# Kernel tuning notes

Hardware: AMD Instinct MI355X
Metric: run time of the kernel (lower is better)

## Reference

```python
import jax, jax.numpy as jnp
import numpy as np

N = 50000          # num_entities
R = 16             # num_relations
D = 128            # embedding_dim
B = 4              # num_blocks
d = D // B         # block size (32)
E = 800000         # num edges


def setup_inputs() -> dict:
    key = jax.random.key(0)
    ks = jax.random.split(key, 9)
    s = 1.0 / np.sqrt(D)
    return {
        "edge_index": jax.random.randint(ks[0], (2, E), 0, N),
        "edge_type": jax.random.randint(ks[1], (E,), 0, R),
        "node_emb": jax.random.normal(ks[2], (N, D), jnp.float32) * s,
        "W1": jax.random.normal(ks[3], (R, B, d, d), jnp.float32) * s,
        "root1": jax.random.normal(ks[4], (D, D), jnp.float32) * s,
        "bias1": jax.random.normal(ks[5], (D,), jnp.float32) * 0.01,
        "W2": jax.random.normal(ks[6], (R, B, d, d), jnp.float32) * s,
        "root2": jax.random.normal(ks[7], (D, D), jnp.float32) * s,
        "bias2": jax.random.normal(ks[8], (D,), jnp.float32) * 0.01,
    }


def _rgcn_conv(x, src, dst, et, W, root, bias):
    # x: [N, D]; W: [R, B, d, d] block-diagonal per-relation weights.
    n = x.shape[0]
    # Transform every node under every relation (cheaper than gathering
    # per-edge weight blocks): [R, N, B, d] -> [R, N, D]
    allR = jnp.einsum('nbi,rbio->rnbo', x.reshape(n, B, d), W).reshape(R, n, D)
    msg = allR[et, src]                                   # [E, D] gather
    # Per-relation mean normalization 1/c_{i,r} (PyG RGCNConv aggr='mean'
    # applied per relation): count edges per (dst, relation) pair.
    seg = dst * R + et
    cnt = jax.ops.segment_sum(jnp.ones_like(et, x.dtype), seg, num_segments=n * R)
    norm = 1.0 / jnp.maximum(cnt[seg], 1.0)               # [E]
    agg = jax.ops.segment_sum(msg * norm[:, None], dst, num_segments=n)
    return agg + x @ root + bias


def reference(edge_index, edge_type, node_emb, W1, root1, bias1, W2, root2, bias2):
    src, dst = edge_index[0], edge_index[1]
    h = _rgcn_conv(node_emb, src, dst, edge_type, W1, root1, bias1)
    h = jax.nn.relu(h)  # dropout is identity in eval mode
    return _rgcn_conv(h, src, dst, edge_type, W2, root2, bias2)
```

## Files before the change

kernel.cpp:

```cpp
#include <hip/hip_runtime.h>
#include <hip/hip_bf16.h>

#define N_NODES 50000
#define N_REL   16
#define DIM     128
#define NBLK    4
#define BS      32
#define N_EDGES 800000
#define NSEG    (N_NODES * N_REL)
#define SCAN_BLK 1024
#define N_SCAN_BLKS ((NSEG + SCAN_BLK - 1) / SCAN_BLK)
#define NWT     (N_NODES / 16)

typedef __attribute__((ext_vector_type(8))) short s8v;
typedef __attribute__((ext_vector_type(8))) unsigned short u8v;
typedef __attribute__((ext_vector_type(4))) float f4v;

__device__ __forceinline__ float bf2f(unsigned short u) {
    return __uint_as_float(((unsigned int)u) << 16);
}
__device__ __forceinline__ unsigned short f2bfbits(float f) {
    unsigned int u = __float_as_uint(f);
    return (unsigned short)((u + 0x7fffu + ((u >> 16) & 1u)) >> 16);
}

__global__ __launch_bounds__(256) void count_kernel(const int* __restrict__ src,
                                                    const int* __restrict__ dst,
                                                    const int* __restrict__ et,
                                                    int* __restrict__ cnt,
                                                    int* __restrict__ used, int E) {
    int e = blockIdx.x * 256 + threadIdx.x;
    if (e < E) {
        int r = et[e];
        atomicAdd(&cnt[dst[e] * N_REL + r], 1);
        used[r * N_NODES + src[e]] = 1;
    }
}

__global__ __launch_bounds__(256) void scan1j_kernel(const int* __restrict__ cnt,
                                                     const int* __restrict__ used,
                                                     int* __restrict__ off,
                                                     int* __restrict__ cmap,
                                                     int2* __restrict__ bsum, int M) {
    const int t = threadIdx.x;
    const int base = blockIdx.x * SCAN_BLK + t * 4;
    int c[4], u[4];
#pragma unroll
    for (int i = 0; i < 4; ++i) {
        int idx = base + i;
        c[i] = (idx < M) ? cnt[idx] : 0;
        u[i] = (idx < M) ? used[idx] : 0;
    }
    int cs = c[0] + c[1] + c[2] + c[3];
    int us = u[0] + u[1] + u[2] + u[3];
    const int lane = t & 63, wid = t >> 6;
    int cinc = cs, uinc = us;
    for (int d = 1; d < 64; d <<= 1) {
        int a = __shfl_up(cinc, d, 64);
        int b = __shfl_up(uinc, d, 64);
        if (lane >= d) { cinc += a; uinc += b; }
    }
    __shared__ int cw[5], uw[5];
    if (lane == 63) { cw[wid] = cinc; uw[wid] = uinc; }
    __syncthreads();
    if (t == 0) {
        int a = 0, b = 0;
        for (int w = 0; w < 4; ++w) {
            int x = cw[w]; cw[w] = a; a += x;
            int y = uw[w]; uw[w] = b; b += y;
        }
        cw[4] = a; uw[4] = b;
    }
    __syncthreads();
    int cex = cinc - cs + cw[wid];
    int uex = uinc - us + uw[wid];
#pragma unroll
    for (int i = 0; i < 4; ++i) {
        int idx = base + i;
        if (idx < M) { off[idx] = cex; cmap[idx] = uex; }
        cex += c[i]; uex += u[i];
    }
    if (t == 0) bsum[blockIdx.x] = make_int2(cw[4], uw[4]);
}

__global__ __launch_bounds__(1024) void scan2j_kernel(int2* __restrict__ bsum, int nb) {
    const int t = threadIdx.x;
    int2 s = (t < nb) ? bsum[t] : make_int2(0, 0);
    const int lane = t & 63, wid = t >> 6;
    int ci = s.x, ui = s.y;
    for (int d = 1; d < 64; d <<= 1) {
        int a = __shfl_up(ci, d, 64);
        int b = __shfl_up(ui, d, 64);
        if (lane >= d) { ci += a; ui += b; }
    }
    __shared__ int cw[16], uw[16];
    if (lane == 63) { cw[wid] = ci; uw[wid] = ui; }
    __syncthreads();
    if (t == 0) {
        int a = 0, b = 0;
        for (int w = 0; w < 16; ++w) {
            int x = cw[w]; cw[w] = a; a += x;
            int y = uw[w]; uw[w] = b; b += y;
        }
    }
    __syncthreads();
    if (t < nb) bsum[t] = make_int2(ci - s.x + cw[wid], ui - s.y + uw[wid]);
}

__global__ __launch_bounds__(256) void scan3j_kernel(int* __restrict__ off,
                                                     int* __restrict__ cmap,
                                                     const int2* __restrict__ bsum, int M) {
    int i = blockIdx.x * 256 + threadIdx.x;
    if (i < M) {
        int2 b = bsum[i / SCAN_BLK];
        off[i] += b.x;
        cmap[i] += b.y;
    }
}

__global__ __launch_bounds__(256) void scatter_fast_kernel(const int* __restrict__ src,
                                                           const int* __restrict__ dst,
                                                           const int* __restrict__ et,
                                                           int* __restrict__ off,
                                                           const int* __restrict__ cnt,
                                                           const int* __restrict__ cmap,
                                                           int2* __restrict__ evec, int E) {
    int e = blockIdx.x * 256 + threadIdx.x;
    if (e < E) {
        int r = et[e];
        int seg = dst[e] * N_REL + r;
        int pos = atomicAdd(&off[seg], 1);
        float inv = 1.0f / (float)cnt[seg];
        int g = cmap[r * N_NODES + src[e]];
        evec[pos] = make_int2(g, __float_as_int(inv));
    }
}

__global__ __launch_bounds__(256) void scan1_kernel(const int* __restrict__ in,
                                                    int* __restrict__ out,
                                                    int* __restrict__ bsum, int M) {
    const int t = threadIdx.x;
    const int base = blockIdx.x * SCAN_BLK + t * 4;
    int v0 = (base + 0 < M) ? in[base + 0] : 0;
    int v1 = (base + 1 < M) ? in[base + 1] : 0;
    int v2 = (base + 2 < M) ? in[base + 2] : 0;
    int v3 = (base + 3 < M) ? in[base + 3] : 0;
    const int s = v0 + v1 + v2 + v3;
    const int lane = t & 63, wid = t >> 6;
    int inc = s;
    for (int d = 1; d < 64; d <<= 1) {
        int u = __shfl_up(inc, d, 64);
        if (lane >= d) inc += u;
    }
    __shared__ int wsum[5];
    if (lane == 63) wsum[wid] = inc;
    __syncthreads();
    if (t == 0) {
        int a = 0;
        for (int w = 0; w < 4; ++w) { int u = wsum[w]; wsum[w] = a; a += u; }
        wsum[4] = a;
    }
    __syncthreads();
    const int ex = inc - s + wsum[wid];
    if (base + 0 < M) out[base + 0] = ex;
    if (base + 1 < M) out[base + 1] = ex + v0;
    if (base + 2 < M) out[base + 2] = ex + v0 + v1;
    if (base + 3 < M) out[base + 3] = ex + v0 + v1 + v2;
    if (t == 0) bsum[blockIdx.x] = wsum[4];
}

__global__ __launch_bounds__(1024) void scan2_kernel(int* __restrict__ bsum, int nb) {
    const int t = threadIdx.x;
    int s = (t < nb) ? bsum[t] : 0;
    const int lane = t & 63, wid = t >> 6;
    int inc = s;
    for (int d = 1; d < 64; d <<= 1) {
        int u = __shfl_up(inc, d, 64);
        if (lane >= d) inc += u;
    }
    __shared__ int wsum[16];
    if (lane == 63) wsum[wid] = inc;
    __syncthreads();
    if (t == 0) {
        int a = 0;
        for (int w = 0; w < 16; ++w) { int u = wsum[w]; wsum[w] = a; a += u; }
    }
    __syncthreads();
    const int ex = inc - s + wsum[wid];
    if (t < nb) bsum[t] = ex;
}

__global__ __launch_bounds__(256) void scan3_kernel(int* __restrict__ out,
                                                    const int* __restrict__ bsum, int M) {
    int i = blockIdx.x * 256 + threadIdx.x;
    if (i < M) out[i] += bsum[i / SCAN_BLK];
}

__global__ __launch_bounds__(256) void scatter_old_kernel(const int* __restrict__ src,
                                                          const int* __restrict__ dst,
                                                          const int* __restrict__ et,
                                                          int* __restrict__ off,
                                                          int* __restrict__ srcs, int E) {
    int e = blockIdx.x * 256 + threadIdx.x;
    if (e < E) {
        int seg = dst[e] * N_REL + et[e];
        int pos = atomicAdd(&off[seg], 1);
        srcs[pos] = src[e];
    }
}

__global__ __launch_bounds__(256) void prep_kernel(const float* __restrict__ W1,
                                                   const float* __restrict__ W2,
                                                   const float* __restrict__ r1,
                                                   const float* __restrict__ r2,
                                                   ushort* __restrict__ WB1,
                                                   ushort* __restrict__ WB2,
                                                   ushort* __restrict__ RB1,
                                                   ushort* __restrict__ RB2) {
    int t = blockIdx.x * 256 + threadIdx.x;
    if (t < 262144) {
        const float* W = (t < 131072) ? W1 : W2;
        ushort* WB     = (t < 131072) ? WB1 : WB2;
        int idx = t & 131071;
        int i  = idx & 7;
        int lm = (idx >> 3) & 15;
        int kg = (idx >> 7) & 3;
        int mt = (idx >> 9) & 1;
        int b  = (idx >> 10) & 3;
        int r  = idx >> 12;
        WB[idx] = f2bfbits(W[((size_t)(r * 4 + b) * 32 + kg * 8 + i) * 32 + mt * 16 + lm]);
    } else if (t < 294912) {
        int u = t - 262144;
        const float* R = (u < 16384) ? r1 : r2;
        ushort* RB     = (u < 16384) ? RB1 : RB2;
        int idx = u & 16383;
        int i  = idx & 7;
        int lm = (idx >> 3) & 15;
        int kg = (idx >> 7) & 3;
        int kc = (idx >> 9) & 3;
        int mt = (idx >> 11) & 7;
        RB[idx] = f2bfbits(R[(size_t)(kc * 32 + kg * 8 + i) * DIM + mt * 16 + lm]);
    }
}

template<bool IN_BF16, bool OUT_BF16, bool RELU>
__global__ __launch_bounds__(256) void fused_kernel(const void* __restrict__ xin,
                                                    const ushort* __restrict__ WB,
                                                    const ushort* __restrict__ RB,
                                                    const float* __restrict__ bias,
                                                    const int* __restrict__ used,
                                                    const int* __restrict__ cmap,
                                                    char* __restrict__ tab,
                                                    float* __restrict__ scl,
                                                    void* __restrict__ outv) {
    const int wv = threadIdx.x >> 6;
    const int l  = threadIdx.x & 63;
    const int wt = blockIdx.x * 4 + wv;
    if (wt >= NWT) return;
    const int rbase = blockIdx.y * 8;
    const int nbase = wt * 16;
    const int lm = l & 15;
    const int kg = l >> 4;
    const int node = nbase + lm;

    s8v bfr[4];
#pragma unroll
    for (int b = 0; b < 4; ++b) {
        if (IN_BF16) {
            const ushort* xp = (const ushort*)xin + (size_t)node * DIM + b * BS + kg * 8;
            u8v u = *(const u8v*)xp;
#pragma unroll
            for (int i = 0; i < 8; ++i) {
                unsigned short us = u[i];
                if (RELU) us = (us & 0x8000u) ? (unsigned short)0 : us;
                bfr[b][i] = (short)us;
            }
        } else {
            const float* xp = (const float*)xin + (size_t)node * DIM + b * BS + kg * 8;
#pragma unroll
            for (int i = 0; i < 8; ++i) {
                float v = xp[i];
                if (RELU) v = fmaxf(v, 0.f);
                bfr[b][i] = (short)f2bfbits(v);
            }
        }
    }

#pragma unroll 2
    for (int ri = 0; ri < 8; ++ri) {
        const int rr = rbase + ri;
        const int grow = rr * N_NODES + node;
        const int flag = used[grow];
        const int cid  = cmap[grow];
        f4v acc[4][2];
#pragma unroll
        for (int b = 0; b < 4; ++b) {
#pragma unroll
            for (int mt = 0; mt < 2; ++mt) {
                s8v afrag = *(const s8v*)&WB[((((rr * 4 + b) * 2 + mt) * 4 + kg) * 16 + lm) * 8];
                f4v z = {0.f, 0.f, 0.f, 0.f};
                acc[b][mt] = __builtin_amdgcn_mfma_f32_16x16x32_bf16(afrag, bfr[b], z, 0, 0, 0);
            }
        }
        float m = 0.f;
#pragma unroll
        for (int b = 0; b < 4; ++b)
#pragma unroll
            for (int mt = 0; mt < 2; ++mt)
#pragma unroll
                for (int j = 0; j < 4; ++j)
                    m = fmaxf(m, fabsf(acc[b][mt][j]));
        m = fmaxf(m, __shfl_xor(m, 16, 64));
        m = fmaxf(m, __shfl_xor(m, 32, 64));
        m = fmaxf(m, 1e-30f);

        if (flag) {
            const float qs = 127.0f / m;
            unsigned int d[8];
#pragma unroll
            for (int b = 0; b < 4; ++b) {
#pragma unroll
                for (int mt = 0; mt < 2; ++mt) {
                    int q0 = __float2int_rn(acc[b][mt][0] * qs);
                    int q1 = __float2int_rn(acc[b][mt][1] * qs);
                    int q2 = __float2int_rn(acc[b][mt][2] * qs);
                    int q3 = __float2int_rn(acc[b][mt][3] * qs);
                    unsigned int t01 = __builtin_amdgcn_perm((unsigned)q1, (unsigned)q0, 0x00000400u);
                    unsigned int t23 = __builtin_amdgcn_perm((unsigned)q3, (unsigned)q2, 0x00000400u);
                    d[b * 2 + mt] = __builtin_amdgcn_perm(t23, t01, 0x05040100u);
                }
            }
            char* gp = tab + (size_t)cid * 128 + kg * 32;
            *(uint4*)gp        = make_uint4(d[0], d[1], d[2], d[3]);
            *(uint4*)(gp + 16) = make_uint4(d[4], d[5], d[6], d[7]);
            if (kg == 0) scl[cid] = m * (1.0f / 127.0f);
        }
    }

    if (blockIdx.y == 0) {
#pragma unroll 2
        for (int mt = 0; mt < 8; ++mt) {
            const int col0 = mt * 16 + kg * 4;
            f4v acc = *(const f4v*)&bias[col0];
#pragma unroll
            for (int kc = 0; kc < 4; ++kc) {
                s8v afrag = *(const s8v*)&RB[(((mt * 4 + kc) * 4 + kg) * 16 + lm) * 8];
                acc = __builtin_amdgcn_mfma_f32_16x16x32_bf16(afrag, bfr[kc], acc, 0, 0, 0);
            }
            if (OUT_BF16) {
                unsigned int p0 = (unsigned int)f2bfbits(acc[0]) |
                                  ((unsigned int)f2bfbits(acc[1]) << 16);
                unsigned int p1 = (unsigned int)f2bfbits(acc[2]) |
                                  ((unsigned int)f2bfbits(acc[3]) << 16);
                *(uint2*)((ushort*)outv + (size_t)node * DIM + col0) = make_uint2(p0, p1);
            } else {
                *(f4v*)((float*)outv + (size_t)node * DIM + col0) = acc;
            }
        }
    }
}

template<bool OUT_BF16>
__global__ __launch_bounds__(256) void agg8_kernel(const int2* __restrict__ evec,
                                                   const int* __restrict__ off,
                                                   const char* __restrict__ tab,
                                                   const float* __restrict__ scl,
                                                   void* __restrict__ outv) {
    const int hw = threadIdx.x >> 5;
    const int o  = threadIdx.x & 31;
    const int v  = blockIdx.x * 8 + hw;

    const int start = (v == 0) ? 0 : off[v * N_REL - 1];
    const int end   = off[v * N_REL + N_REL - 1];

    const int p = o >> 4;
    const int w = o & 15;

    float acc[8];
#pragma unroll
    for (int j = 0; j < 8; ++j) acc[j] = 0.f;

#pragma unroll 2
    for (int base = start; base < end; base += 4) {
        const int k0 = base + p;
        const int k1 = base + 2 + p;
        const int2 e0 = evec[min(k0, end - 1)];
        const int2 e1 = evec[min(k1, end - 1)];
        const int g0 = e0.x, g1 = e1.x;
        const float i0 = (k0 < end) ? __int_as_float(e0.y) : 0.f;
        const float i1 = (k1 < end) ? __int_as_float(e1.y) : 0.f;
        const uint2 q0 = *(const uint2*)(tab + (size_t)g0 * 128 + w * 8);
        const uint2 q1 = *(const uint2*)(tab + (size_t)g1 * 128 + w * 8);
        const float s0 = scl[g0] * i0;
        const float s1 = scl[g1] * i1;
#pragma unroll
        for (int j = 0; j < 4; ++j) {
            acc[j]     = fmaf((float)(int)(signed char)(q0.x >> (8 * j)), s0, acc[j]);
            acc[4 + j] = fmaf((float)(int)(signed char)(q0.y >> (8 * j)), s0, acc[4 + j]);
        }
#pragma unroll
        for (int j = 0; j < 4; ++j) {
            acc[j]     = fmaf((float)(int)(signed char)(q1.x >> (8 * j)), s1, acc[j]);
            acc[4 + j] = fmaf((float)(int)(signed char)(q1.y >> (8 * j)), s1, acc[4 + j]);
        }
    }
#pragma unroll
    for (int j = 0; j < 8; ++j)
        acc[j] += __shfl_xor(acc[j], 16, 32);

    if (o < 16) {
        const int base0 = (o & 3) * 32 + (o >> 2) * 4;
        if (OUT_BF16) {
            ushort* hp = (ushort*)outv + (size_t)v * DIM + base0;
            ushort4 a0 = *(ushort4*)hp;
            ushort4 a1 = *(ushort4*)(hp + 16);
            a0.x = f2bfbits(bf2f(a0.x) + acc[0]);
            a0.y = f2bfbits(bf2f(a0.y) + acc[1]);
            a0.z = f2bfbits(bf2f(a0.z) + acc[2]);
            a0.w = f2bfbits(bf2f(a0.w) + acc[3]);
            a1.x = f2bfbits(bf2f(a1.x) + acc[4]);
            a1.y = f2bfbits(bf2f(a1.y) + acc[5]);
            a1.z = f2bfbits(bf2f(a1.z) + acc[6]);
            a1.w = f2bfbits(bf2f(a1.w) + acc[7]);
            *(ushort4*)hp        = a0;
            *(ushort4*)(hp + 16) = a1;
        } else {
            float* op = (float*)outv + (size_t)v * DIM + base0;
            float4 r0 = *(float4*)op;
            float4 r1 = *(float4*)(op + 16);
            r0.x += acc[0]; r0.y += acc[1]; r0.z += acc[2]; r0.w += acc[3];
            r1.x += acc[4]; r1.y += acc[5]; r1.z += acc[6]; r1.w += acc[7];
            *(float4*)op        = r0;
            *(float4*)(op + 16) = r1;
        }
    }
}

template<bool RELU>
__global__ __launch_bounds__(256) void dense_old_kernel(const float* __restrict__ x,
                                                        const float* __restrict__ root,
                                                        const float* __restrict__ bias,
                                                        float* __restrict__ out) {
    const int wv = threadIdx.x >> 6;
    const int l  = threadIdx.x & 63;
    const int wt = blockIdx.x * 4 + wv;
    if (wt >= NWT) return;
    const int nbase = wt * 16;
    const int lm = l & 15;
    const int kg = l >> 4;
    const int node = nbase + lm;

    s8v bfr[4];
#pragma unroll
    for (int kc = 0; kc < 4; ++kc) {
        const float* xp = &x[(size_t)node * DIM + kc * BS + kg * 8];
#pragma unroll
        for (int i = 0; i < 8; ++i) {
            float v = xp[i];
            if (RELU) v = fmaxf(v, 0.f);
            bfr[kc][i] = (short)f2bfbits(v);
        }
    }
#pragma unroll 2
    for (int mt = 0; mt < 8; ++mt) {
        const int col0 = mt * 16 + kg * 4;
        f4v acc = *(const f4v*)&bias[col0];
#pragma unroll
        for (int kc = 0; kc < 4; ++kc) {
            const float* rp = &root[(size_t)(kc * BS + kg * 8) * DIM + mt * 16 + lm];
            s8v afrag;
#pragma unroll
            for (int i = 0; i < 8; ++i)
                afrag[i] = (short)f2bfbits(rp[i * DIM]);
            acc = __builtin_amdgcn_mfma_f32_16x16x32_bf16(afrag, bfr[kc], acc, 0, 0, 0);
        }
        *(f4v*)&out[(size_t)node * DIM + col0] = acc;
    }
}

template<bool RELU>
__global__ __launch_bounds__(256) void agg_fallback_kernel(const int* __restrict__ srcs,
                                                           const int* __restrict__ off,
                                                           const int* __restrict__ cnt,
                                                           const float* __restrict__ x,
                                                           const float* __restrict__ W,
                                                           float* __restrict__ out) {
    __shared__ float Wsh[N_REL * BS * BS];
    const int bblk = blockIdx.y;
    for (int idx = threadIdx.x * 4; idx < N_REL * BS * BS; idx += 1024) {
        int r = idx >> 10, rest = idx & 1023;
        *(float4*)&Wsh[idx] = *(const float4*)&W[(r * NBLK + bblk) * 1024 + rest];
    }
    __syncthreads();
    const int hw = threadIdx.x >> 5;
    const int o  = threadIdx.x & 31;
    const int v  = blockIdx.x * 8 + hw;
    int endv = 0, cv = 0;
    if (o < N_REL) { endv = off[v * N_REL + o]; cv = cnt[v * N_REL + o]; }
    float acc = out[v * DIM + bblk * BS + o];
    for (int r = 0; r < N_REL; ++r) {
        const int c = __shfl(cv, r, 32);
        if (c == 0) continue;
        const int end = __shfl(endv, r, 32);
        float xs = 0.f;
        for (int k = end - c; k < end; ++k) {
            const int s = srcs[k];
            float xv = x[s * DIM + bblk * BS + o];
            if (RELU) xv = fmaxf(xv, 0.f);
            xs += xv;
        }
        xs *= (1.0f / (float)c);
        const float* wr = &Wsh[r * (BS * BS)];
#pragma unroll
        for (int i = 0; i < BS; i += 2) {
            float xi0 = __shfl(xs, i, 32);
            float xi1 = __shfl(xs, i + 1, 32);
            acc = fmaf(xi0, wr[i * BS + o], acc);
            acc = fmaf(xi1, wr[(i + 1) * BS + o], acc);
        }
    }
    out[v * DIM + bblk * BS + o] = acc;
}

extern "C" void kernel_launch(void* const* d_in, const int* in_sizes, int n_in,
                              void* d_out, int out_size, void* d_ws, size_t ws_size,
                              hipStream_t stream) {
    const int*   edge_index = (const int*)d_in[0];
    const int*   src   = edge_index;
    const int*   dstv  = edge_index + N_EDGES;
    const int*   et    = (const int*)d_in[1];
    const float* x0    = (const float*)d_in[2];
    const float* W1    = (const float*)d_in[3];
    const float* root1 = (const float*)d_in[4];
    const float* bias1 = (const float*)d_in[5];
    const float* W2    = (const float*)d_in[6];
    const float* root2 = (const float*)d_in[7];
    const float* bias2 = (const float*)d_in[8];
    float* out = (float*)d_out;

    char* ws = (char*)d_ws;
    ushort* h    = (ushort*)ws;
    int*    cnt  = (int*)   (ws + 12800000);
    int*    used = (int*)   (ws + 16000000);
    int*    off  = (int*)   (ws + 19200000);
    int*    cmap = (int*)   (ws + 22400000);
    int2*   evec = (int2*)  (ws + 25600000);
    int2*   bsum = (int2*)  (ws + 32000000);
    ushort* WB1  = (ushort*)(ws + 32008192);
    ushort* WB2  = (ushort*)(ws + 32270336);
    ushort* RB1  = (ushort*)(ws + 32532480);
    ushort* RB2  = (ushort*)(ws + 32565248);
    float*  scl  = (float*) (ws + 32598016);
    char*   tab  =          (ws + 35798016);
    const size_t FAST_NEED = 138198016ull;

    const int egrid = (N_EDGES + 255) / 256;
    const int tgrid = (NWT + 3) / 4;

    if (ws_size >= FAST_NEED) {
        prep_kernel<<<1152, 256, 0, stream>>>(W1, W2, root1, root2, WB1, WB2, RB1, RB2);
        hipMemsetAsync(cnt, 0, 2 * (size_t)NSEG * sizeof(int), stream);
        count_kernel<<<egrid, 256, 0, stream>>>(src, dstv, et, cnt, used, N_EDGES);
        scan1j_kernel<<<N_SCAN_BLKS, 256, 0, stream>>>(cnt, used, off, cmap, bsum, NSEG);
        scan2j_kernel<<<1, 1024, 0, stream>>>(bsum, N_SCAN_BLKS);
        scan3j_kernel<<<(NSEG + 255) / 256, 256, 0, stream>>>(off, cmap, bsum, NSEG);
        scatter_fast_kernel<<<egrid, 256, 0, stream>>>(src, dstv, et, off, cnt, cmap,
                                                       evec, N_EDGES);

        dim3 fgrid(tgrid, 2);
        const int ngrid = N_NODES / 8;

        fused_kernel<false, true, false><<<fgrid, 256, 0, stream>>>(
            x0, WB1, RB1, bias1, used, cmap, tab, scl, h);
        agg8_kernel<true><<<ngrid, 256, 0, stream>>>(evec, off, tab, scl, h);

        fused_kernel<true, false, true><<<fgrid, 256, 0, stream>>>(
            h, WB2, RB2, bias2, used, cmap, tab, scl, out);
        agg8_kernel<false><<<ngrid, 256, 0, stream>>>(evec, off, tab, scl, out);
    } else {
        float* hf    = (float*)d_ws;
        int*   cntf  = (int*)((char*)d_ws + 25600000);
        int*   offf  = (int*)((char*)d_ws + 28800000);
        int*   srcsf = (int*)((char*)d_ws + 32000000);
        int*   bsumf = (int*)((char*)d_ws + 35200000);
        int*   usedD = offf;

        hipMemsetAsync(cntf, 0, (size_t)NSEG * sizeof(int), stream);
        count_kernel<<<egrid, 256, 0, stream>>>(src, dstv, et, cntf, usedD, N_EDGES);
        scan1_kernel<<<N_SCAN_BLKS, 256, 0, stream>>>(cntf, offf, bsumf, NSEG);
        scan2_kernel<<<1, 1024, 0, stream>>>(bsumf, N_SCAN_BLKS);
        scan3_kernel<<<(NSEG + 255) / 256, 256, 0, stream>>>(offf, bsumf, NSEG);
        scatter_old_kernel<<<egrid, 256, 0, stream>>>(src, dstv, et, offf, srcsf, N_EDGES);

        dim3 fgrid2(N_NODES / 8, NBLK);
        dense_old_kernel<false><<<tgrid, 256, 0, stream>>>(x0, root1, bias1, hf);
        agg_fallback_kernel<false><<<fgrid2, 256, 0, stream>>>(srcsf, offf, cntf, x0, W1, hf);
        dense_old_kernel<true><<<tgrid, 256, 0, stream>>>(hf, root2, bias2, out);
        agg_fallback_kernel<true><<<fgrid2, 256, 0, stream>>>(srcsf, offf, cntf, hf, W2, out);
    }
}
```

Baseline: 246.2 us.

## Compact relation transforms to used (relation,node) rows via row-source index

The scan pass now records, for each compacted (relation,node) row, its source node. The fused transform kernel launches one grid slice per relation that iterates only over used rows, plus an extra slice for the root/bias transform. This avoids computing relation transforms for unused pairs and makes table writes contiguous. In exchange, node features are gathered and reloaded once per relation instead of once per half of the relations, which raises read traffic.

Measured after the change: 267.6 us. +8.7%, slower.

```diff
diff --git a/kernel.cpp b/kernel.cpp
--- a/kernel.cpp
+++ b/kernel.cpp
@@ -109,12 +109,16 @@
 
 __global__ __launch_bounds__(256) void scan3j_kernel(int* __restrict__ off,
                                                      int* __restrict__ cmap,
+                                                     const int* __restrict__ used,
+                                                     int* __restrict__ rowsrc,
                                                      const int2* __restrict__ bsum, int M) {
     int i = blockIdx.x * 256 + threadIdx.x;
     if (i < M) {
         int2 b = bsum[i / SCAN_BLK];
         off[i] += b.x;
-        cmap[i] += b.y;
+        int cm = cmap[i] + b.y;
+        cmap[i] = cm;
+        if (used[i]) rowsrc[cm] = i - (i / N_NODES) * N_NODES;
     }
 }
 
@@ -244,60 +248,61 @@
 }
 
 template<bool IN_BF16, bool OUT_BF16, bool RELU>
-__global__ __launch_bounds__(256) void fused_kernel(const void* __restrict__ xin,
-                                                    const ushort* __restrict__ WB,
-                                                    const ushort* __restrict__ RB,
-                                                    const float* __restrict__ bias,
-                                                    const int* __restrict__ used,
-                                                    const int* __restrict__ cmap,
-                                                    char* __restrict__ tab,
-                                                    float* __restrict__ scl,
-                                                    void* __restrict__ outv) {
+__global__ __launch_bounds__(256) void fused2_kernel(const void* __restrict__ xin,
+                                                     const ushort* __restrict__ WB,
+                                                     const ushort* __restrict__ RB,
+                                                     const float* __restrict__ bias,
+                                                     const int* __restrict__ used,
+                                                     const int* __restrict__ cmap,
+                                                     const int* __restrict__ rowsrc,
+                                                     char* __restrict__ tab,
+                                                     float* __restrict__ scl,
+                                                     void* __restrict__ outv) {
     const int wv = threadIdx.x >> 6;
     const int l  = threadIdx.x & 63;
-    const int wt = blockIdx.x * 4 + wv;
-    if (wt >= NWT) return;
-    const int rbase = blockIdx.y * 8;
-    const int nbase = wt * 16;
     const int lm = l & 15;
     const int kg = l >> 4;
-    const int node = nbase + lm;
-
-    s8v bfr[4];
-#pragma unroll
-    for (int b = 0; b < 4; ++b) {
-        if (IN_BF16) {
-            const ushort* xp = (const ushort*)xin + (size_t)node * DIM + b * BS + kg * 8;
-            u8v u = *(const u8v*)xp;
-#pragma unroll
-            for (int i = 0; i < 8; ++i) {
-                unsigned short us = u[i];
-                if (RELU) us = (us & 0x8000u) ? (unsigned short)0 : us;
-                bfr[b][i] = (short)us;
+    const int y  = blockIdx.y;
+
+    if (y < N_REL) {
+        const int sr = cmap[(size_t)y * N_NODES];
+        const int er = (y < N_REL - 1) ? cmap[(size_t)(y + 1) * N_NODES]
+                                       : (cmap[NSEG - 1] + used[NSEG - 1]);
+        const int row0 = sr + (blockIdx.x * 4 + wv) * 16;
+        if (row0 >= er) return;
+        const int row    = row0 + lm;
+        const bool active = (row < er);
+        const int node = rowsrc[active ? row : (er - 1)];
+
+        s8v bfr[4];
+#pragma unroll
+        for (int b = 0; b < 4; ++b) {
+            if (IN_BF16) {
+                const ushort* xp = (const ushort*)xin + (size_t)node * DIM + b * BS + kg * 8;
+                u8v u = *(const u8v*)xp;
+#pragma unroll
+                for (int i = 0; i < 8; ++i) {
+                    unsigned short us = u[i];
+                    if (RELU) us = (us & 0x8000u) ? (unsigned short)0 : us;
+                    bfr[b][i] = (short)us;
+                }
+            } else {
+                const float* xp = (const float*)xin + (size_t)node * DIM + b * BS + kg * 8;
+#pragma unroll
+                for (int i = 0; i < 8; ++i) {
+                    float v = xp[i];
+                    if (RELU) v = fmaxf(v, 0.f);
+                    bfr[b][i] = (short)f2bfbits(v);
+                }
             }
-        } else {
-            const float* xp = (const float*)xin + (size_t)node * DIM + b * BS + kg * 8;
-#pragma unroll
-            for (int i = 0; i < 8; ++i) {
-                float v = xp[i];
-                if (RELU) v = fmaxf(v, 0.f);
-                bfr[b][i] = (short)f2bfbits(v);
-            }
-        }
-    }
-
-#pragma unroll 2
-    for (int ri = 0; ri < 8; ++ri) {
-        const int rr = rbase + ri;
-        const int grow = rr * N_NODES + node;
-        const int flag = used[grow];
-        const int cid  = cmap[grow];
+        }
+
         f4v acc[4][2];
 #pragma unroll
         for (int b = 0; b < 4; ++b) {
 #pragma unroll
             for (int mt = 0; mt < 2; ++mt) {
-                s8v afrag = *(const s8v*)&WB[((((rr * 4 + b) * 2 + mt) * 4 + kg) * 16 + lm) * 8];
+                s8v afrag = *(const s8v*)&WB[((((y * 4 + b) * 2 + mt) * 4 + kg) * 16 + lm) * 8];
                 f4v z = {0.f, 0.f, 0.f, 0.f};
                 acc[b][mt] = __builtin_amdgcn_mfma_f32_16x16x32_bf16(afrag, bfr[b], z, 0, 0, 0);
             }
@@ -313,49 +318,74 @@
         m = fmaxf(m, __shfl_xor(m, 16, 64));
         m = fmaxf(m, __shfl_xor(m, 32, 64));
         m = fmaxf(m, 1e-30f);
-
-        if (flag) {
-            const float qs = 127.0f / m;
-            unsigned int d[8];
-#pragma unroll
-            for (int b = 0; b < 4; ++b) {
-#pragma unroll
-                for (int mt = 0; mt < 2; ++mt) {
-                    int q0 = __float2int_rn(acc[b][mt][0] * qs);
-                    int q1 = __float2int_rn(acc[b][mt][1] * qs);
-                    int q2 = __float2int_rn(acc[b][mt][2] * qs);
-                    int q3 = __float2int_rn(acc[b][mt][3] * qs);
-                    unsigned int t01 = __builtin_amdgcn_perm((unsigned)q1, (unsigned)q0, 0x00000400u);
-                    unsigned int t23 = __builtin_amdgcn_perm((unsigned)q3, (unsigned)q2, 0x00000400u);
-                    d[b * 2 + mt] = __builtin_amdgcn_perm(t23, t01, 0x05040100u);
-                }
+        const float qs = 127.0f / m;
+
+        unsigned int d[8];
+#pragma unroll
+        for (int b = 0; b < 4; ++b) {
+#pragma unroll
+            for (int mt = 0; mt < 2; ++mt) {
+                int q0 = __float2int_rn(acc[b][mt][0] * qs);
+                int q1 = __float2int_rn(acc[b][mt][1] * qs);
+                int q2 = __float2int_rn(acc[b][mt][2] * qs);
+                int q3 = __float2int_rn(acc[b][mt][3] * qs);
+                unsigned int t01 = __builtin_amdgcn_perm((unsigned)q1, (unsigned)q0, 0x00000400u);
+                unsigned int t23 = __builtin_amdgcn_perm((unsigned)q3, (unsigned)q2, 0x00000400u);
+                d[b * 2 + mt] = __builtin_amdgcn_perm(t23, t01, 0x05040100u);
             }
-            char* gp = tab + (size_t)cid * 128 + kg * 32;
+        }
+        if (active) {
+            char* gp = tab + (size_t)row * 128 + kg * 32;
             *(uint4*)gp        = make_uint4(d[0], d[1], d[2], d[3]);
             *(uint4*)(gp + 16) = make_uint4(d[4], d[5], d[6], d[7]);
-            if (kg == 0) scl[cid] = m * (1.0f / 127.0f);
-        }
-    }
-
-    if (blockIdx.y == 0) {
+            if (kg == 0) scl[row] = m * (1.0f / 127.0f);
+        }
+        return;
+    }
+
+    const int wt = blockIdx.x * 4 + wv;
+    if (wt >= NWT) return;
+    const int node = wt * 16 + lm;
+
+    s8v bfr[4];
+#pragma unroll
+    for (int kc = 0; kc < 4; ++kc) {
+        if (IN_BF16) {
+            const ushort* xp = (const ushort*)xin + (size_t)node * DIM + kc * BS + kg * 8;
+            u8v u = *(const u8v*)xp;
+#pragma unroll
+            for (int i = 0; i < 8; ++i) {
+                unsigned short us = u[i];
+                if (RELU) us = (us & 0x8000u) ? (unsigned short)0 : us;
+                bfr[kc][i] = (short)us;
+            }
+        } else {
+            const float* xp = (const float*)xin + (size_t)node * DIM + kc * BS + kg * 8;
+#pragma unroll
+            for (int i = 0; i < 8; ++i) {
+                float v = xp[i];
+                if (RELU) v = fmaxf(v, 0.f);
+                bfr[kc][i] = (short)f2bfbits(v);
+            }
+        }
+    }
 #pragma unroll 2
-        for (int mt = 0; mt < 8; ++mt) {
-            const int col0 = mt * 16 + kg * 4;
-            f4v acc = *(const f4v*)&bias[col0];
-#pragma unroll
-            for (int kc = 0; kc < 4; ++kc) {
-                s8v afrag = *(const s8v*)&RB[(((mt * 4 + kc) * 4 + kg) * 16 + lm) * 8];
-                acc = __builtin_amdgcn_mfma_f32_16x16x32_bf16(afrag, bfr[kc], acc, 0, 0, 0);
-            }
-            if (OUT_BF16) {
-                unsigned int p0 = (unsigned int)f2bfbits(acc[0]) |
-                                  ((unsigned int)f2bfbits(acc[1]) << 16);
-                unsigned int p1 = (unsigned int)f2bfbits(acc[2]) |
-                                  ((unsigned int)f2bfbits(acc[3]) << 16);
-                *(uint2*)((ushort*)outv + (size_t)node * DIM + col0) = make_uint2(p0, p1);
-            } else {
-                *(f4v*)((float*)outv + (size_t)node * DIM + col0) = acc;
-            }
+    for (int mt = 0; mt < 8; ++mt) {
+        const int col0 = mt * 16 + kg * 4;
+        f4v acc = *(const f4v*)&bias[col0];
+#pragma unroll
+        for (int kc = 0; kc < 4; ++kc) {
+            s8v afrag = *(const s8v*)&RB[(((mt * 4 + kc) * 4 + kg) * 16 + lm) * 8];
+            acc = __builtin_amdgcn_mfma_f32_16x16x32_bf16(afrag, bfr[kc], acc, 0, 0, 0);
+        }
+        if (OUT_BF16) {
+            unsigned int p0 = (unsigned int)f2bfbits(acc[0]) |
+                              ((unsigned int)f2bfbits(acc[1]) << 16);
+            unsigned int p1 = (unsigned int)f2bfbits(acc[2]) |
+                              ((unsigned int)f2bfbits(acc[3]) << 16);
+            *(uint2*)((ushort*)outv + (size_t)node * DIM + col0) = make_uint2(p0, p1);
+        } else {
+            *(f4v*)((float*)outv + (size_t)node * DIM + col0) = acc;
         }
     }
 }
@@ -539,20 +569,21 @@
     float* out = (float*)d_out;
 
     char* ws = (char*)d_ws;
-    ushort* h    = (ushort*)ws;
-    int*    cnt  = (int*)   (ws + 12800000);
-    int*    used = (int*)   (ws + 16000000);
-    int*    off  = (int*)   (ws + 19200000);
-    int*    cmap = (int*)   (ws + 22400000);
-    int2*   evec = (int2*)  (ws + 25600000);
-    int2*   bsum = (int2*)  (ws + 32000000);
-    ushort* WB1  = (ushort*)(ws + 32008192);
-    ushort* WB2  = (ushort*)(ws + 32270336);
-    ushort* RB1  = (ushort*)(ws + 32532480);
-    ushort* RB2  = (ushort*)(ws + 32565248);
-    float*  scl  = (float*) (ws + 32598016);
-    char*   tab  =          (ws + 35798016);
-    const size_t FAST_NEED = 138198016ull;
+    ushort* h      = (ushort*)ws;
+    int*    cnt    = (int*)   (ws + 12800000);
+    int*    used   = (int*)   (ws + 16000000);
+    int*    off    = (int*)   (ws + 19200000);
+    int*    cmap   = (int*)   (ws + 22400000);
+    int2*   evec   = (int2*)  (ws + 25600000);
+    int2*   bsum   = (int2*)  (ws + 32000000);
+    ushort* WB1    = (ushort*)(ws + 32008192);
+    ushort* WB2    = (ushort*)(ws + 32270336);
+    ushort* RB1    = (ushort*)(ws + 32532480);
+    ushort* RB2    = (ushort*)(ws + 32565248);
+    float*  scl    = (float*) (ws + 32598016);
+    int*    rowsrc = (int*)   (ws + 35798016);
+    char*   tab    =          (ws + 38998016);
+    const size_t FAST_NEED = 141398016ull;
 
     const int egrid = (N_EDGES + 255) / 256;
     const int tgrid = (NWT + 3) / 4;
@@ -563,19 +594,20 @@
         count_kernel<<<egrid, 256, 0, stream>>>(src, dstv, et, cnt, used, N_EDGES);
         scan1j_kernel<<<N_SCAN_BLKS, 256, 0, stream>>>(cnt, used, off, cmap, bsum, NSEG);
         scan2j_kernel<<<1, 1024, 0, stream>>>(bsum, N_SCAN_BLKS);
-        scan3j_kernel<<<(NSEG + 255) / 256, 256, 0, stream>>>(off, cmap, bsum, NSEG);
+        scan3j_kernel<<<(NSEG + 255) / 256, 256, 0, stream>>>(off, cmap, used, rowsrc,
+                                                              bsum, NSEG);
         scatter_fast_kernel<<<egrid, 256, 0, stream>>>(src, dstv, et, off, cnt, cmap,
                                                        evec, N_EDGES);
 
-        dim3 fgrid(tgrid, 2);
+        dim3 fgrid(tgrid, N_REL + 1);
         const int ngrid = N_NODES / 8;
 
-        fused_kernel<false, true, false><<<fgrid, 256, 0, stream>>>(
-            x0, WB1, RB1, bias1, used, cmap, tab, scl, h);
+        fused2_kernel<false, true, false><<<fgrid, 256, 0, stream>>>(
+            x0, WB1, RB1, bias1, used, cmap, rowsrc, tab, scl, h);
         agg8_kernel<true><<<ngrid, 256, 0, stream>>>(evec, off, tab, scl, h);
 
-        fused_kernel<true, false, true><<<fgrid, 256, 0, stream>>>(
-            h, WB2, RB2, bias2, used, cmap, tab, scl, out);
+        fused2_kernel<true, false, true><<<fgrid, 256, 0, stream>>>(
+            h, WB2, RB2, bias2, used, cmap, rowsrc, tab, scl, out);
         agg8_kernel<false><<<ngrid, 256, 0, stream>>>(evec, off, tab, scl, out);
     } else {
         float* hf    = (float*)d_ws;
```
